# Kernel optimization log

Hardware: AMD Instinct MI355X
Metric: run time of the kernel (lower is better)

The kernel has to match this reference:

```python
import jax, jax.numpy as jnp
import numpy as np

WIN_FRONT = 6
WIN_BACK = 3
LN_EPS = 1e-3  # keras LayerNormalization default epsilon

B, T, D = 2, 2048, 512
H, DH = 8, 64  # num_heads, head_size


def chunk_mask(T):
    # Faithful port of _compute_chunk_mask; True = attend allowed.
    i = jnp.arange(T)[:, None]
    j = jnp.arange(T)[None, :]
    low = jnp.maximum(i - WIN_FRONT, 0)
    high = jnp.clip(i + WIN_BACK, 0, T)
    low = low - jnp.maximum(low - T + WIN_BACK, 0)
    high = high + jnp.maximum(WIN_BACK - high, 0)
    return (j >= low) & (j <= high)  # [T, T] bool


def setup_inputs() -> dict:
    key = jax.random.key(0)
    ks = jax.random.split(key, 12)
    s = 0.02
    return {
        "x": jax.random.normal(ks[0], (B, T, D), jnp.float32),
        "gamma": jnp.ones((D,), jnp.float32),
        "beta": jnp.zeros((D,), jnp.float32),
        "Wq": jax.random.normal(ks[1], (D, H, DH), jnp.float32) * s,
        "bq": jnp.zeros((H, DH), jnp.float32),
        "Wk": jax.random.normal(ks[2], (D, H, DH), jnp.float32) * s,
        "bk": jnp.zeros((H, DH), jnp.float32),
        "Wv": jax.random.normal(ks[3], (D, H, DH), jnp.float32) * s,
        "bv": jnp.zeros((H, DH), jnp.float32),
        "Wo": jax.random.normal(ks[4], (H, DH, D), jnp.float32) * s,
        "bo": jnp.zeros((D,), jnp.float32),
    }


def reference(x, gamma, beta, Wq, bq, Wk, bk, Wv, bv, Wo, bo):
    T_ = x.shape[1]
    mask = chunk_mask(T_)  # [T, T] bool, broadcast over batch/heads

    # LayerNorm (eps=1e-3 as keras default)
    mu = jnp.mean(x, axis=-1, keepdims=True)
    var = jnp.var(x, axis=-1, keepdims=True)
    h = (x - mu) * jax.lax.rsqrt(var + LN_EPS) * gamma + beta

    # MultiHeadAttention (keras): q/k/v projections with bias
    q = jnp.einsum('btd,dhk->bthk', h, Wq) + bq
    k = jnp.einsum('bsd,dhk->bshk', h, Wk) + bk
    v = jnp.einsum('bsd,dhk->bshk', h, Wv) + bv

    scores = jnp.einsum('bthk,bshk->bhts', q, k) / jnp.sqrt(jnp.asarray(DH, h.dtype))
    neg = jnp.asarray(-1e9, scores.dtype)
    scores = jnp.where(mask[None, None], scores, neg)
    attn = jax.nn.softmax(scores, axis=-1)

    ctx = jnp.einsum('bhts,bshk->bthk', attn, v)
    out = jnp.einsum('bthk,hkd->btd', ctx, Wo) + bo

    return x + out  # residual add (dropout=0, inference)
```

## Files before the change

### kernel.cpp

```cpp
#include <hip/hip_runtime.h>
#include <hip/hip_bf16.h>

#define B_ 2
#define T_ 2048
#define D_ 512
#define H_ 8
#define DH_ 64
#define NROW 4096
#define NQKV 1536

typedef __bf16 bf16x8 __attribute__((ext_vector_type(8)));
typedef float f32x4 __attribute__((ext_vector_type(4)));

__device__ __forceinline__ unsigned short f2bf(float f) {
  unsigned int u = __float_as_uint(f);
  unsigned int r = (u + 0x7fffu + ((u >> 16) & 1u)) >> 16;
  return (unsigned short)r;
}
__device__ __forceinline__ float bf2f(unsigned short s) {
  return __uint_as_float(((unsigned int)s) << 16);
}

__device__ __forceinline__ void gload_lds16(const void* g, void* l) {
  __builtin_amdgcn_global_load_lds(
      (__attribute__((address_space(1))) void*)(void*)(g),
      (__attribute__((address_space(3))) void*)(l), 16, 0, 0);
}

__global__ __launch_bounds__(256) void prep_kernel(
    const float* __restrict__ Wq, const float* __restrict__ Wk,
    const float* __restrict__ Wv, const float* __restrict__ Wo,
    const float* __restrict__ bq, const float* __restrict__ bk,
    const float* __restrict__ bv,
    unsigned short* __restrict__ Wt,
    unsigned short* __restrict__ Wot,
    float* __restrict__ bias_cat)
{
  const int bid = blockIdx.x;
  const int tid = threadIdx.x;
  if (bid == 256) {
    for (int i = tid; i < NQKV; i += 256) {
      const float* s = (i < 512) ? bq : ((i < 1024) ? bk : bv);
      bias_cat[i] = s[i & 511];
    }
    return;
  }
  __shared__ unsigned short tile[64][66];
  const int mat = bid >> 6;
  const int tb = bid & 63;
  const int tn = tb >> 3, tk = tb & 7;
  const int k0 = tk << 6, n0 = tn << 6;
  const float* src = (mat == 0) ? Wq : (mat == 1) ? Wk : (mat == 2) ? Wv : Wo;
  unsigned short* dst = (mat < 3) ? (Wt + (size_t)mat * 512 * 512) : Wot;

  #pragma unroll
  for (int p = 0; p < 16; ++p) {
    int e = (p << 8) + tid;
    int kr = e >> 6, nc = e & 63;
    tile[kr][nc] = f2bf(src[(size_t)(k0 + kr) * 512 + n0 + nc]);
  }
  __syncthreads();
  #pragma unroll
  for (int p = 0; p < 16; ++p) {
    int e = (p << 8) + tid;
    int nr = e >> 6, kc = e & 63;
    dst[(size_t)(n0 + nr) * 512 + k0 + kc] = tile[kc][nr];
  }
}

__global__ __launch_bounds__(256) void ln_kernel(
    const float* __restrict__ x, const float* __restrict__ gamma,
    const float* __restrict__ beta, unsigned short* __restrict__ h)
{
  const int lane = threadIdx.x & 63;
  const int row = (blockIdx.x << 2) + (threadIdx.x >> 6);
  const float* xr = x + (size_t)row * D_ + lane * 8;
  float4 v0 = *(const float4*)xr;
  float4 v1 = *(const float4*)(xr + 4);
  float xv[8] = {v0.x, v0.y, v0.z, v0.w, v1.x, v1.y, v1.z, v1.w};
  float s = 0.f, ss = 0.f;
  #pragma unroll
  for (int i = 0; i < 8; ++i) { s += xv[i]; ss += xv[i] * xv[i]; }
  #pragma unroll
  for (int off = 32; off > 0; off >>= 1) {
    s  += __shfl_xor(s, off);
    ss += __shfl_xor(ss, off);
  }
  float mu  = s * (1.0f / D_);
  float var = ss * (1.0f / D_) - mu * mu;
  float rs  = rsqrtf(var + 1e-3f);
  const float* gp = gamma + lane * 8;
  const float* bp = beta + lane * 8;
  float4 g0 = *(const float4*)gp;
  float4 g1 = *(const float4*)(gp + 4);
  float4 b0 = *(const float4*)bp;
  float4 b1 = *(const float4*)(bp + 4);
  float gv[8] = {g0.x, g0.y, g0.z, g0.w, g1.x, g1.y, g1.z, g1.w};
  float bv8[8] = {b0.x, b0.y, b0.z, b0.w, b1.x, b1.y, b1.z, b1.w};
  unsigned int pk[4];
  #pragma unroll
  for (int i = 0; i < 4; ++i) {
    unsigned short lo = f2bf((xv[2*i]   - mu) * rs * gv[2*i]   + bv8[2*i]);
    unsigned short hi = f2bf((xv[2*i+1] - mu) * rs * gv[2*i+1] + bv8[2*i+1]);
    pk[i] = (unsigned int)lo | ((unsigned int)hi << 16);
  }
  uint4 out4 = make_uint4(pk[0], pk[1], pk[2], pk[3]);
  *(uint4*)(h + (size_t)row * D_ + lane * 8) = out4;
}

template<int EPI>
__global__ __launch_bounds__(256) void gemm_bf16(
    const unsigned short* __restrict__ A,
    const unsigned short* __restrict__ Bt,
    const float* __restrict__ bias,
    const float* __restrict__ resid,
    void* __restrict__ outp,
    int M, int N, int K)
{
  __shared__ unsigned short Asm[2][128 * 32];
  __shared__ unsigned short Bsm[2][128 * 32];
  const int tid = threadIdx.x;
  const int lane = tid & 63;
  const int w = tid >> 6;
  const int m0 = blockIdx.y << 7;
  const int n0 = blockIdx.x << 7;
  const int wr = w >> 1, wc = w & 1;

  f32x4 acc[4][4];
  #pragma unroll
  for (int m = 0; m < 4; ++m)
    #pragma unroll
    for (int n = 0; n < 4; ++n) acc[m][n] = f32x4{0.f, 0.f, 0.f, 0.f};

  const int frow = lane & 15;
  const int fk = (lane >> 4) << 3;

  const int cbase0 = (w << 1) << 6;
  const int cbase1 = ((w << 1) + 1) << 6;
  const int c0 = cbase0 + lane;
  const int c1 = cbase1 + lane;

  #define STAGE(k0, buf)                                                     \
    do {                                                                     \
      gload_lds16(A  + (size_t)(m0 + (c0 >> 2)) * K + (k0) + ((c0 & 3) << 3),\
                  (char*)Asm[buf] + cbase0 * 16);                            \
      gload_lds16(Bt + (size_t)(n0 + (c0 >> 2)) * K + (k0) + ((c0 & 3) << 3),\
                  (char*)Bsm[buf] + cbase0 * 16);                            \
      gload_lds16(A  + (size_t)(m0 + (c1 >> 2)) * K + (k0) + ((c1 & 3) << 3),\
                  (char*)Asm[buf] + cbase1 * 16);                            \
      gload_lds16(Bt + (size_t)(n0 + (c1 >> 2)) * K + (k0) + ((c1 & 3) << 3),\
                  (char*)Bsm[buf] + cbase1 * 16);                            \
    } while (0)

  STAGE(0, 0);
  __syncthreads();

  const int NT = K >> 5;
  for (int t = 0; t < NT; ++t) {
    const int cur = t & 1;
    if (t + 1 < NT) STAGE((t + 1) << 5, cur ^ 1);
    bf16x8 a[4], b[4];
    #pragma unroll
    for (int m = 0; m < 4; ++m)
      a[m] = *(const bf16x8*)&Asm[cur][((wr << 6) + (m << 4) + frow) * 32 + fk];
    #pragma unroll
    for (int n = 0; n < 4; ++n)
      b[n] = *(const bf16x8*)&Bsm[cur][((wc << 6) + (n << 4) + frow) * 32 + fk];
    #pragma unroll
    for (int m = 0; m < 4; ++m)
      #pragma unroll
      for (int n = 0; n < 4; ++n)
        acc[m][n] = __builtin_amdgcn_mfma_f32_16x16x32_bf16(a[m], b[n], acc[m][n], 0, 0, 0);
    __syncthreads();
  }
  #undef STAGE

  const int rbase = m0 + (wr << 6) + ((lane >> 4) << 2);
  const int cbase = n0 + (wc << 6) + (lane & 15);
  #pragma unroll
  for (int m = 0; m < 4; ++m) {
    #pragma unroll
    for (int n = 0; n < 4; ++n) {
      const int cc = cbase + (n << 4);
      const float bs = bias[cc];
      #pragma unroll
      for (int r = 0; r < 4; ++r) {
        const int rr = rbase + (m << 4) + r;
        const float val = acc[m][n][r] + bs;
        if (EPI == 1) {
          ((unsigned short*)outp)[(size_t)rr * N + cc] = f2bf(val);
        } else {
          const size_t o = (size_t)rr * N + cc;
          ((float*)outp)[o] = val + resid[o];
        }
      }
    }
  }
}

__global__ __launch_bounds__(256) void attn_kernel(
    const unsigned short* __restrict__ qkv,
    unsigned short* __restrict__ ctx)
{
  __shared__ float qs[64][65];
  __shared__ float ks[80][65];
  __shared__ float vs[80][64];
  __shared__ float ssm[64][12];
  __shared__ float ps[64][12];
  const int tid = threadIdx.x;
  const int bx = blockIdx.x;
  const int chunk = bx & 31;
  const int hh = (bx >> 5) & 7;
  const int bb = bx >> 8;
  const int t0 = chunk << 6;
  const size_t base_bt = (size_t)(bb * T_) * NQKV + hh * 64;

  for (int e = tid; e < 64 * 64; e += 256) {
    int i = e >> 6, d = e & 63;
    qs[i][d] = bf2f(qkv[base_bt + (size_t)(t0 + i) * NQKV + d]);
  }
  for (int e = tid; e < 80 * 64; e += 256) {
    int i = e >> 6, d = e & 63;
    int tt = t0 - 6 + i;
    bool ok = (tt >= 0) && (tt < T_);
    if (ok) {
      size_t idx = base_bt + (size_t)tt * NQKV + d;
      ks[i][d] = bf2f(qkv[idx + 512]);
      vs[i][d] = bf2f(qkv[idx + 1024]);
    } else {
      ks[i][d] = 0.f;
      vs[i][d] = 0.f;
    }
  }
  __syncthreads();

  for (int e = tid; e < 640; e += 256) {
    int tl = e / 10, j = e - tl * 10;
    int tk = t0 + tl - 6 + j;
    float sc = -1e30f;
    if (tk >= 0 && tk < T_) {
      float a = 0.f;
      #pragma unroll
      for (int d = 0; d < 64; ++d) a += qs[tl][d] * ks[tl + j][d];
      sc = a * 0.125f;
    }
    ssm[tl][j] = sc;
  }
  __syncthreads();

  if (tid < 64) {
    float mx = -1e30f;
    #pragma unroll
    for (int j = 0; j < 10; ++j) mx = fmaxf(mx, ssm[tid][j]);
    float sum = 0.f;
    float e10[10];
    #pragma unroll
    for (int j = 0; j < 10; ++j) { e10[j] = __expf(ssm[tid][j] - mx); sum += e10[j]; }
    float inv = 1.0f / sum;
    #pragma unroll
    for (int j = 0; j < 10; ++j) ps[tid][j] = e10[j] * inv;
  }
  __syncthreads();

  for (int e = tid; e < 64 * 64; e += 256) {
    int tl = e >> 6, d = e & 63;
    float a = 0.f;
    #pragma unroll
    for (int j = 0; j < 10; ++j) a += ps[tl][j] * vs[tl + j][d];
    ctx[(size_t)(bb * T_ + t0 + tl) * D_ + hh * 64 + d] = f2bf(a);
  }
}

extern "C" void kernel_launch(void* const* d_in, const int* in_sizes, int n_in,
                              void* d_out, int out_size, void* d_ws, size_t ws_size,
                              hipStream_t stream) {
  const float* x     = (const float*)d_in[0];
  const float* gamma = (const float*)d_in[1];
  const float* beta  = (const float*)d_in[2];
  const float* Wq    = (const float*)d_in[3];
  const float* bq    = (const float*)d_in[4];
  const float* Wk    = (const float*)d_in[5];
  const float* bk    = (const float*)d_in[6];
  const float* Wv    = (const float*)d_in[7];
  const float* bv    = (const float*)d_in[8];
  const float* Wo    = (const float*)d_in[9];
  const float* bo    = (const float*)d_in[10];
  float* out = (float*)d_out;

  char* ws = (char*)d_ws;
  unsigned short* h   = (unsigned short*)(ws);
  unsigned short* Wt  = (unsigned short*)(ws + 4194304);
  unsigned short* Wot = (unsigned short*)(ws + 5767168);
  float* bias_cat     = (float*)(ws + 6291456);
  unsigned short* qkv = (unsigned short*)(ws + 6297600);
  unsigned short* ctx = (unsigned short*)(ws + 6297600 + 12582912);

  prep_kernel<<<257, 256, 0, stream>>>(Wq, Wk, Wv, Wo, bq, bk, bv, Wt, Wot, bias_cat);
  ln_kernel<<<1024, 256, 0, stream>>>(x, gamma, beta, h);
  gemm_bf16<1><<<dim3(12, 32), 256, 0, stream>>>(h, Wt, bias_cat, nullptr, qkv, NROW, NQKV, D_);
  attn_kernel<<<512, 256, 0, stream>>>(qkv, ctx);
  gemm_bf16<2><<<dim3(4, 32), 256, 0, stream>>>(ctx, Wot, bo, x, out, NROW, D_, D_);
}
```

Baseline: 129.9 us.

## Fuse weight prep with LayerNorm and narrow GEMM N-tile to 64

Merges the weight transpose/convert kernel and the LayerNorm kernel into a single launch, with block ranges selecting the role, which saves one kernel launch. The GEMM is templated on its N-tile width and both projections now use 128x64 tiles, doubling grid size (768 and 256 blocks) to fill the 256 CUs better. The cost is less operand reuse per block and more A-tile reloads.

```diff
diff --git a/kernel.cpp b/kernel.cpp
--- a/kernel.cpp
+++ b/kernel.cpp
@@ -27,17 +27,44 @@
       (__attribute__((address_space(3))) void*)(l), 16, 0, 0);
 }
 
-__global__ __launch_bounds__(256) void prep_kernel(
+__global__ __launch_bounds__(256) void prep_ln_kernel(
     const float* __restrict__ Wq, const float* __restrict__ Wk,
     const float* __restrict__ Wv, const float* __restrict__ Wo,
     const float* __restrict__ bq, const float* __restrict__ bk,
     const float* __restrict__ bv,
+    const float* __restrict__ x, const float* __restrict__ gamma,
+    const float* __restrict__ beta,
     unsigned short* __restrict__ Wt,
     unsigned short* __restrict__ Wot,
-    float* __restrict__ bias_cat)
+    float* __restrict__ bias_cat,
+    unsigned short* __restrict__ h)
 {
   const int bid = blockIdx.x;
   const int tid = threadIdx.x;
+  __shared__ unsigned short tile[64][66];
+
+  if (bid < 256) {
+    const int mat = bid >> 6;
+    const int tb = bid & 63;
+    const int tn = tb >> 3, tk = tb & 7;
+    const int k0 = tk << 6, n0 = tn << 6;
+    const float* src = (mat == 0) ? Wq : (mat == 1) ? Wk : (mat == 2) ? Wv : Wo;
+    unsigned short* dst = (mat < 3) ? (Wt + (size_t)mat * 512 * 512) : Wot;
+    #pragma unroll
+    for (int p = 0; p < 16; ++p) {
+      int e = (p << 8) + tid;
+      int kr = e >> 6, nc = e & 63;
+      tile[kr][nc] = f2bf(src[(size_t)(k0 + kr) * 512 + n0 + nc]);
+    }
+    __syncthreads();
+    #pragma unroll
+    for (int p = 0; p < 16; ++p) {
+      int e = (p << 8) + tid;
+      int nr = e >> 6, kc = e & 63;
+      dst[(size_t)(n0 + nr) * 512 + k0 + kc] = tile[kc][nr];
+    }
+    return;
+  }
   if (bid == 256) {
     for (int i = tid; i < NQKV; i += 256) {
       const float* s = (i < 512) ? bq : ((i < 1024) ? bk : bv);
@@ -45,35 +72,8 @@
     }
     return;
   }
-  __shared__ unsigned short tile[64][66];
-  const int mat = bid >> 6;
-  const int tb = bid & 63;
-  const int tn = tb >> 3, tk = tb & 7;
-  const int k0 = tk << 6, n0 = tn << 6;
-  const float* src = (mat == 0) ? Wq : (mat == 1) ? Wk : (mat == 2) ? Wv : Wo;
-  unsigned short* dst = (mat < 3) ? (Wt + (size_t)mat * 512 * 512) : Wot;
-
-  #pragma unroll
-  for (int p = 0; p < 16; ++p) {
-    int e = (p << 8) + tid;
-    int kr = e >> 6, nc = e & 63;
-    tile[kr][nc] = f2bf(src[(size_t)(k0 + kr) * 512 + n0 + nc]);
-  }
-  __syncthreads();
-  #pragma unroll
-  for (int p = 0; p < 16; ++p) {
-    int e = (p << 8) + tid;
-    int nr = e >> 6, kc = e & 63;
-    dst[(size_t)(n0 + nr) * 512 + k0 + kc] = tile[kc][nr];
-  }
-}
-
-__global__ __launch_bounds__(256) void ln_kernel(
-    const float* __restrict__ x, const float* __restrict__ gamma,
-    const float* __restrict__ beta, unsigned short* __restrict__ h)
-{
-  const int lane = threadIdx.x & 63;
-  const int row = (blockIdx.x << 2) + (threadIdx.x >> 6);
+  const int lane = tid & 63;
+  const int row = ((bid - 257) << 2) + (tid >> 6);
   const float* xr = x + (size_t)row * D_ + lane * 8;
   float4 v0 = *(const float4*)xr;
   float4 v1 = *(const float4*)(xr + 4);
@@ -108,7 +108,7 @@
   *(uint4*)(h + (size_t)row * D_ + lane * 8) = out4;
 }
 
-template<int EPI>
+template<int EPI, int BN>
 __global__ __launch_bounds__(256) void gemm_bf16(
     const unsigned short* __restrict__ A,
     const unsigned short* __restrict__ Bt,
@@ -117,70 +117,76 @@
     void* __restrict__ outp,
     int M, int N, int K)
 {
+  constexpr int NF = BN / 32;
+  constexpr int WAVE_N = BN / 2;
   __shared__ unsigned short Asm[2][128 * 32];
-  __shared__ unsigned short Bsm[2][128 * 32];
+  __shared__ unsigned short Bsm[2][BN * 32];
   const int tid = threadIdx.x;
   const int lane = tid & 63;
   const int w = tid >> 6;
   const int m0 = blockIdx.y << 7;
-  const int n0 = blockIdx.x << 7;
+  const int n0 = blockIdx.x * BN;
   const int wr = w >> 1, wc = w & 1;
 
-  f32x4 acc[4][4];
+  f32x4 acc[4][NF];
   #pragma unroll
   for (int m = 0; m < 4; ++m)
     #pragma unroll
-    for (int n = 0; n < 4; ++n) acc[m][n] = f32x4{0.f, 0.f, 0.f, 0.f};
+    for (int n = 0; n < NF; ++n) acc[m][n] = f32x4{0.f, 0.f, 0.f, 0.f};
 
   const int frow = lane & 15;
   const int fk = (lane >> 4) << 3;
 
-  const int cbase0 = (w << 1) << 6;
-  const int cbase1 = ((w << 1) + 1) << 6;
-  const int c0 = cbase0 + lane;
-  const int c1 = cbase1 + lane;
-
-  #define STAGE(k0, buf)                                                     \
-    do {                                                                     \
-      gload_lds16(A  + (size_t)(m0 + (c0 >> 2)) * K + (k0) + ((c0 & 3) << 3),\
-                  (char*)Asm[buf] + cbase0 * 16);                            \
-      gload_lds16(Bt + (size_t)(n0 + (c0 >> 2)) * K + (k0) + ((c0 & 3) << 3),\
-                  (char*)Bsm[buf] + cbase0 * 16);                            \
-      gload_lds16(A  + (size_t)(m0 + (c1 >> 2)) * K + (k0) + ((c1 & 3) << 3),\
-                  (char*)Asm[buf] + cbase1 * 16);                            \
-      gload_lds16(Bt + (size_t)(n0 + (c1 >> 2)) * K + (k0) + ((c1 & 3) << 3),\
-                  (char*)Bsm[buf] + cbase1 * 16);                            \
-    } while (0)
-
-  STAGE(0, 0);
+  const int ca0 = (w << 7);
+  const int ca1 = ca0 + 64;
+  const int c0 = ca0 + lane;
+  const int c1 = ca1 + lane;
+  const int cb0 = (w << 6) + lane;
+
+  auto stage = [&](int k0, int buf) {
+    gload_lds16(A + (size_t)(m0 + (c0 >> 2)) * K + k0 + ((c0 & 3) << 3),
+                (char*)Asm[buf] + ca0 * 16);
+    gload_lds16(A + (size_t)(m0 + (c1 >> 2)) * K + k0 + ((c1 & 3) << 3),
+                (char*)Asm[buf] + ca1 * 16);
+    if constexpr (BN == 128) {
+      gload_lds16(Bt + (size_t)(n0 + (c0 >> 2)) * K + k0 + ((c0 & 3) << 3),
+                  (char*)Bsm[buf] + ca0 * 16);
+      gload_lds16(Bt + (size_t)(n0 + (c1 >> 2)) * K + k0 + ((c1 & 3) << 3),
+                  (char*)Bsm[buf] + ca1 * 16);
+    } else {
+      gload_lds16(Bt + (size_t)(n0 + (cb0 >> 2)) * K + k0 + ((cb0 & 3) << 3),
+                  (char*)Bsm[buf] + (w << 6) * 16);
+    }
+  };
+
+  stage(0, 0);
   __syncthreads();
 
   const int NT = K >> 5;
   for (int t = 0; t < NT; ++t) {
     const int cur = t & 1;
-    if (t + 1 < NT) STAGE((t + 1) << 5, cur ^ 1);
-    bf16x8 a[4], b[4];
+    if (t + 1 < NT) stage((t + 1) << 5, cur ^ 1);
+    bf16x8 a[4], b[NF];
     #pragma unroll
     for (int m = 0; m < 4; ++m)
       a[m] = *(const bf16x8*)&Asm[cur][((wr << 6) + (m << 4) + frow) * 32 + fk];
     #pragma unroll
-    for (int n = 0; n < 4; ++n)
-      b[n] = *(const bf16x8*)&Bsm[cur][((wc << 6) + (n << 4) + frow) * 32 + fk];
+    for (int n = 0; n < NF; ++n)
+      b[n] = *(const bf16x8*)&Bsm[cur][(wc * WAVE_N + (n << 4) + frow) * 32 + fk];
     #pragma unroll
     for (int m = 0; m < 4; ++m)
       #pragma unroll
-      for (int n = 0; n < 4; ++n)
+      for (int n = 0; n < NF; ++n)
         acc[m][n] = __builtin_amdgcn_mfma_f32_16x16x32_bf16(a[m], b[n], acc[m][n], 0, 0, 0);
     __syncthreads();
   }
-  #undef STAGE
 
   const int rbase = m0 + (wr << 6) + ((lane >> 4) << 2);
-  const int cbase = n0 + (wc << 6) + (lane & 15);
+  const int cbase = n0 + wc * WAVE_N + (lane & 15);
   #pragma unroll
   for (int m = 0; m < 4; ++m) {
     #pragma unroll
-    for (int n = 0; n < 4; ++n) {
+    for (int n = 0; n < NF; ++n) {
       const int cc = cbase + (n << 4);
       const float bs = bias[cc];
       #pragma unroll
@@ -295,9 +301,9 @@
   unsigned short* qkv = (unsigned short*)(ws + 6297600);
   unsigned short* ctx = (unsigned short*)(ws + 6297600 + 12582912);
 
-  prep_kernel<<<257, 256, 0, stream>>>(Wq, Wk, Wv, Wo, bq, bk, bv, Wt, Wot, bias_cat);
-  ln_kernel<<<1024, 256, 0, stream>>>(x, gamma, beta, h);
-  gemm_bf16<1><<<dim3(12, 32), 256, 0, stream>>>(h, Wt, bias_cat, nullptr, qkv, NROW, NQKV, D_);
+  prep_ln_kernel<<<1281, 256, 0, stream>>>(Wq, Wk, Wv, Wo, bq, bk, bv,
+                                           x, gamma, beta, Wt, Wot, bias_cat, h);
+  gemm_bf16<1, 64><<<dim3(24, 32), 256, 0, stream>>>(h, Wt, bias_cat, nullptr, qkv, NROW, NQKV, D_);
   attn_kernel<<<512, 256, 0, stream>>>(qkv, ctx);
-  gemm_bf16<2><<<dim3(4, 32), 256, 0, stream>>>(ctx, Wot, bo, x, out, NROW, D_, D_);
-}
+  gemm_bf16<2, 64><<<dim3(8, 32), 256, 0, stream>>>(ctx, Wot, bo, x, out, NROW, D_, D_);
+}
```

Result: faster. 123.9 us (-4.6%).
